# Kernel optimization log

Measured on AMD Instinct MI355X. Metric: run time of the kernel, lower is better.

## Reference

```python
import jax, jax.numpy as jnp
import numpy as np

B, L, D = 4, 2048, 512
N_HEAD, D_K, D_V = 8, 64, 64
D_INNER, N_LAYERS, NUM_TYPES = 2048, 4, 22
PAD = 0
LN_EPS = 1e-6


def _layer_norm(x, g, b):
    m = jnp.mean(x, axis=-1, keepdims=True)
    v = jnp.mean((x - m) ** 2, axis=-1, keepdims=True)
    return (x - m) * jax.lax.rsqrt(v + LN_EPS) * g + b


def _temporal_enc(time, non_pad_mask):
    # position_vec[i] = 10000^(2*(i//2)/d_model)
    i = np.arange(D)
    pos_vec = jnp.asarray(10000.0 ** (2.0 * (i // 2) / D), dtype=jnp.float32)
    r = time[:, :, None] / pos_vec                      # [B,L,D]
    even = (jnp.arange(D) % 2) == 0
    r = jnp.where(even, jnp.sin(r), jnp.cos(r))
    return r * non_pad_mask


def setup_inputs() -> dict:
    key = jax.random.key(0)
    ks = jax.random.split(key, 20)
    event_type = jax.random.randint(ks[0], (B, L), 0, NUM_TYPES + 1)
    event_time = jnp.cumsum(jax.random.uniform(ks[1], (B, L), dtype=jnp.float32), axis=1)
    non_pad_mask = (event_type != PAD).astype(jnp.float32)[:, :, None]
    s = 0.02
    emb = jax.random.normal(ks[2], (NUM_TYPES + 1, D), dtype=jnp.float32) * s
    emb = emb.at[PAD].set(0.0)  # padding_idx row
    Wq = jax.random.normal(ks[3], (N_LAYERS, D, N_HEAD * D_K), dtype=jnp.float32) * s
    Wk = jax.random.normal(ks[4], (N_LAYERS, D, N_HEAD * D_K), dtype=jnp.float32) * s
    Wv = jax.random.normal(ks[5], (N_LAYERS, D, N_HEAD * D_V), dtype=jnp.float32) * s
    fc_w = jax.random.normal(ks[6], (N_LAYERS, N_HEAD * D_V, D), dtype=jnp.float32) * s
    fc_b = jnp.zeros((N_LAYERS, D), dtype=jnp.float32)
    ln1_g = jnp.ones((N_LAYERS, D), dtype=jnp.float32)
    ln1_b = jnp.zeros((N_LAYERS, D), dtype=jnp.float32)
    W1 = jax.random.normal(ks[7], (N_LAYERS, D, D_INNER), dtype=jnp.float32) * s
    b1 = jnp.zeros((N_LAYERS, D_INNER), dtype=jnp.float32)
    W2 = jax.random.normal(ks[8], (N_LAYERS, D_INNER, D), dtype=jnp.float32) * s
    b2 = jnp.zeros((N_LAYERS, D), dtype=jnp.float32)
    ln2_g = jnp.ones((N_LAYERS, D), dtype=jnp.float32)
    ln2_b = jnp.zeros((N_LAYERS, D), dtype=jnp.float32)
    return dict(event_type=event_type, event_time=event_time, non_pad_mask=non_pad_mask,
                emb=emb, Wq=Wq, Wk=Wk, Wv=Wv, fc_w=fc_w, fc_b=fc_b,
                ln1_g=ln1_g, ln1_b=ln1_b, W1=W1, b1=b1, W2=W2, b2=b2,
                ln2_g=ln2_g, ln2_b=ln2_b)


def reference(event_type, event_time, non_pad_mask, emb, Wq, Wk, Wv, fc_w, fc_b,
              ln1_g, ln1_b, W1, b1, W2, b2, ln2_g, ln2_b):
    # Attention mask. NOTE: in the source, slf_attn_mask_sparse is overwritten by
    # the keypad mask, so the effective mask is padding | causal.
    pad = (event_type == PAD)                                   # [B,L]
    keypad = pad[:, None, :]                                    # [B,1(L_q),L_k] broadcast
    subseq = jnp.triu(jnp.ones((L, L), dtype=bool), k=1)        # [L,L]
    mask = (keypad | subseq)[:, None, :, :]                     # [B,1,L,L] over heads

    tem = _temporal_enc(event_time, non_pad_mask)               # [B,L,D]
    x = emb[event_type]                                         # [B,L,D]
    scale = 1.0 / jnp.sqrt(jnp.float32(D_K))

    for l in range(N_LAYERS):
        x = x + tem
        # --- multi-head attention (post-LN, THP style) ---
        residual = x
        q = (x @ Wq[l]).reshape(B, L, N_HEAD, D_K)
        k = (x @ Wk[l]).reshape(B, L, N_HEAD, D_K)
        v = (x @ Wv[l]).reshape(B, L, N_HEAD, D_V)
        scores = jnp.einsum('bqhd,bkhd->bhqk', q, k) * scale    # [B,H,L,L]
        scores = jnp.where(mask, -1e9, scores)
        attn = jax.nn.softmax(scores, axis=-1)
        out = jnp.einsum('bhqk,bkhd->bqhd', attn, v).reshape(B, L, N_HEAD * D_V)
        out = out @ fc_w[l] + fc_b[l] + residual
        x = _layer_norm(out, ln1_g[l], ln1_b[l])
        x = x * non_pad_mask
        # --- position-wise FFN (exact GELU, post-LN) ---
        residual = x
        h = jax.nn.gelu(x @ W1[l] + b1[l], approximate=False)
        y = h @ W2[l] + b2[l] + residual
        x = _layer_norm(y, ln2_g[l], ln2_b[l])
        x = x * non_pad_mask
    return x
```

## Files before the change

kernel.cpp:

```cpp
#include <hip/hip_runtime.h>
#include <math.h>

#define BB 4
#define LL 2048
#define DD 512
#define NH 8
#define DINNER 2048
#define NLAYERS 4
#define MM (BB * LL)

typedef __attribute__((ext_vector_type(8))) __bf16 bf16x8;
typedef __attribute__((ext_vector_type(4))) float f32x4;
typedef __attribute__((ext_vector_type(4))) unsigned short us4;

__device__ __forceinline__ unsigned short f2b(float f) {
  union { __bf16 h; unsigned short u; } v;
  v.h = (__bf16)f;
  return v.u;
}
__device__ __forceinline__ float b2f(unsigned short h) {
  union { unsigned u; float f; } v; v.u = ((unsigned)h) << 16; return v.f;
}
__device__ __forceinline__ unsigned pk2(float lo, float hi) {
  return (unsigned)f2b(lo) | ((unsigned)f2b(hi) << 16);
}
__device__ __forceinline__ float exp2f_fast(float x) {
  float r; asm("v_exp_f32 %0, %1" : "=v"(r) : "v"(x)); return r;
}

__device__ __forceinline__ void gload16(const void* g, void* l) {
  __builtin_amdgcn_global_load_lds(
      (const __attribute__((address_space(1))) void*)g,
      (__attribute__((address_space(3))) void*)l, 16, 0, 0);
}

__global__ __launch_bounds__(512) void init_kernel(
    const int* __restrict__ etype, const float* __restrict__ etime,
    const float* __restrict__ npm, const float* __restrict__ emb,
    float* __restrict__ tem, float* __restrict__ xa,
    unsigned short* __restrict__ xab) {
  int row = blockIdx.x;
  int d = threadIdx.x;
  float t = etime[row];
  float mask = npm[row];
  int dd = d & ~1;
  float pv = expf(9.210340371976184f * ((float)dd * (1.0f / (float)DD)));
  float r = t / pv;
  float val = (d & 1) ? cosf(r) : sinf(r);
  float tv = val * mask;
  tem[(size_t)row * DD + d] = tv;
  int ty = etype[row];
  float a = emb[(size_t)ty * DD + d] + tv;
  xa[(size_t)row * DD + d] = a;
  xab[(size_t)row * DD + d] = f2b(a);
}

__global__ __launch_bounds__(256) void wtrans_kernel(
    const float* __restrict__ in, unsigned short* __restrict__ out,
    int K, int N, long in_ls, long out_ls) {
  __shared__ float t[32][33];
  int l = blockIdx.z;
  int n0 = blockIdx.x * 32, k0 = blockIdx.y * 32;
  int tx = threadIdx.x & 31, ty = threadIdx.x >> 5;
  const float* ip = in + (size_t)l * in_ls;
  unsigned short* op = out + (size_t)l * out_ls;
#pragma unroll
  for (int r = ty; r < 32; r += 8)
    t[r][tx] = ip[(size_t)(k0 + r) * N + n0 + tx];
  __syncthreads();
#pragma unroll
  for (int r = ty; r < 32; r += 8)
    op[(size_t)(n0 + r) * K + k0 + tx] = f2b(t[tx][r]);
}

template <int BM, int BN, bool BIAS, bool RES, bool GELU_, bool OBF16>
__global__ __launch_bounds__(256) void gemm_kernel(
    const unsigned short* __restrict__ A, const unsigned short* __restrict__ WT,
    const float* __restrict__ bias, const float* __restrict__ res, int ldres,
    void* __restrict__ Cv, int ldc, int M, int N, int K) {
  __shared__ unsigned short As[2][BM * 32];
  __shared__ unsigned short Bs[2][BN * 32];
  constexpr int MT = (BM == 128) ? 4 : ((BN == 64) ? 2 : 4);
  constexpr int NT = (BM == 128 && BN == 128) ? 4 : 2;
  int tid = threadIdx.x;
  int w = tid >> 6, l = tid & 63;
  int li = l & 15, g = l >> 4;
  int nwg = gridDim.x;
  int bid = blockIdx.x;
  int wg = (bid & 7) * (nwg >> 3) + (bid >> 3);
  int gx = N / BN;
  int row0 = (wg / gx) * BM, col0 = (wg % gx) * BN;
  int wm = (BM == 128) ? (w & 1) * 64 : ((BN == 64) ? (w >> 1) * 32 : 0);
  int wnb = (BM == 128) ? (w >> 1) * 64 : ((BN == 64) ? (w & 1) * 32 : w * 32);
  f32x4 acc[MT][NT];
#pragma unroll
  for (int i = 0; i < MT; i++)
#pragma unroll
    for (int j = 0; j < NT; j++) acc[i][j] = (f32x4){0.f, 0.f, 0.f, 0.f};

  int lr = l >> 2;
  int lc = (l & 3) ^ (lr & 3);

  auto stage = [&](int bb, int kb) {
    int k0 = kb * 32;
    if (BM == 128) {
#pragma unroll
      for (int i = 0; i < 2; i++) {
        int ai = w * 2 + i;
        gload16(A + (size_t)(row0 + ai * 16 + lr) * K + k0 + lc * 8,
                &As[bb][ai * 512]);
      }
    } else {
      gload16(A + (size_t)(row0 + w * 16 + lr) * K + k0 + lc * 8,
              &As[bb][w * 512]);
    }
    if (BN == 128) {
#pragma unroll
      for (int i = 0; i < 2; i++) {
        int bi = w * 2 + i;
        gload16(WT + (size_t)(col0 + bi * 16 + lr) * K + k0 + lc * 8,
                &Bs[bb][bi * 512]);
      }
    } else {
      gload16(WT + (size_t)(col0 + w * 16 + lr) * K + k0 + lc * 8,
              &Bs[bb][w * 512]);
    }
  };

  int nk = K >> 5;
  stage(0, 0);
  __syncthreads();
  int buf = 0;
  for (int kb = 0; kb < nk; kb++) {
    if (kb + 1 < nk) stage(buf ^ 1, kb + 1);
    bf16x8 af[MT], bf_[NT];
#pragma unroll
    for (int mt = 0; mt < MT; mt++) {
      int r = wm + mt * 16 + li;
      af[mt] = *(const bf16x8*)&As[buf][r * 32 + ((g ^ (r & 3)) * 8)];
    }
#pragma unroll
    for (int nt = 0; nt < NT; nt++) {
      int r = wnb + nt * 16 + li;
      bf_[nt] = *(const bf16x8*)&Bs[buf][r * 32 + ((g ^ (r & 3)) * 8)];
    }
#pragma unroll
    for (int mt = 0; mt < MT; mt++)
#pragma unroll
      for (int nt = 0; nt < NT; nt++)
        acc[mt][nt] = __builtin_amdgcn_mfma_f32_16x16x32_bf16(
            af[mt], bf_[nt], acc[mt][nt], 0, 0, 0);
    __syncthreads();
    buf ^= 1;
  }
#pragma unroll
  for (int mt = 0; mt < MT; mt++) {
#pragma unroll
    for (int nt = 0; nt < NT; nt++) {
#pragma unroll
      for (int r = 0; r < 4; r++) {
        int row = row0 + wm + mt * 16 + g * 4 + r;
        int col = col0 + wnb + nt * 16 + li;
        float v = acc[mt][nt][r];
        if (BIAS) v += bias[col];
        if (RES) v += res[(size_t)row * ldres + col];
        if (GELU_) v = 0.5f * v * (1.0f + erff(v * 0.70710678118654752f));
        if (OBF16)
          ((unsigned short*)Cv)[(size_t)row * ldc + col] = f2b(v);
        else
          ((float*)Cv)[(size_t)row * ldc + col] = v;
      }
    }
  }
}

__global__ __launch_bounds__(256) void vtrans_kernel(
    const unsigned short* __restrict__ qkv, unsigned short* __restrict__ vT) {
  __shared__ unsigned short t[64][65];
  int bh = blockIdx.y;
  int b = bh >> 3, h = bh & 7;
  int l0 = blockIdx.x * 64;
  int tid = threadIdx.x;
  int c = tid & 63, p = tid >> 6;
#pragma unroll
  for (int r = p; r < 64; r += 4)
    t[r][c] = qkv[(size_t)(b * LL + l0 + r) * 1536 + 1024 + h * 64 + c];
  __syncthreads();
#pragma unroll
  for (int r = p; r < 64; r += 4)
    vT[((size_t)bh * 64 + r) * LL + l0 + c] = t[c][r];
}

__global__ __launch_bounds__(256) void meanv_kernel(
    const unsigned short* __restrict__ vT, float* __restrict__ meanVpart) {
  __shared__ float red[4][64];
  int chunk = blockIdx.x & 7;
  int bh = blockIdx.x >> 3;
  int tid = threadIdx.x;
  int d = tid & 63, p = tid >> 6;
  const unsigned short* vp =
      vT + ((size_t)bh * 64 + d) * LL + chunk * 256 + p * 64;
  float s = 0.f;
#pragma unroll
  for (int i = 0; i < 16; i++) {
    us4 v = *(const us4*)&vp[i * 4];
    s += b2f(v[0]) + b2f(v[1]) + b2f(v[2]) + b2f(v[3]);
  }
  red[p][d] = s;
  __syncthreads();
  if (p == 0)
    meanVpart[(size_t)blockIdx.x * 64 + d] =
        red[0][d] + red[1][d] + red[2][d] + red[3][d];
}

__global__ __launch_bounds__(256) void attn_kernel(
    const unsigned short* __restrict__ qkv, const unsigned short* __restrict__ vT,
    const int* __restrict__ etype, unsigned short* __restrict__ opart,
    float* __restrict__ ml) {
  __shared__ unsigned short Ks[2][64 * 64];
  __shared__ unsigned short Ps[64][72];
  int hwbid = blockIdx.x;
  int work = (hwbid & 7) * 256 + (hwbid >> 3);
  int bh = work >> 6;
  int rem = work & 63;
  int qt = 31 - (rem >> 1);
  int half = rem & 1;
  int h = bh & 7, b = bh >> 3;
  int q0 = qt * 64;
  int nt = qt + 1;
  int ha = (nt + 1) >> 1;
  int j0 = half ? ha : 0;
  int j1 = half ? nt : ha;
  int pidx = (bh * 32 + qt) * 2 + half;
  int tid = threadIdx.x, w = tid >> 6, l = tid & 63;
  int g = l >> 4, li = l & 15;
  const float SC = 0.125f * 1.44269504f;

  f32x4 o[4];
#pragma unroll
  for (int n = 0; n < 4; n++) o[n] = (f32x4){0.f, 0.f, 0.f, 0.f};
  float mreg[4], lreg[4];
#pragma unroll
  for (int r = 0; r < 4; r++) { mreg[r] = -3.0e38f; lreg[r] = 0.f; }

  if (j0 < j1) {
    const unsigned short* qrp =
        qkv + (size_t)(b * LL + q0 + w * 16 + li) * 1536 + h * 64;
    bf16x8 aq0 = *(const bf16x8*)&qrp[g * 8];
    bf16x8 aq1 = *(const bf16x8*)&qrp[32 + g * 8];

#pragma unroll
    for (int e = 0; e < 2; e++) {
      int idx = e * 256 + tid;
      int r = idx >> 3;
      int src = (l & 7) ^ (r & 7);
      gload16(
          qkv + (size_t)(b * LL + j0 * 64 + r) * 1536 + 512 + h * 64 + src * 8,
          &Ks[0][(e * 256 + w * 64) * 8]);
    }
    __syncthreads();

    int cur = 0;
    for (int j = j0; j < j1; j++) {
      int k0 = j << 6;
      if (j + 1 < j1) {
#pragma unroll
        for (int e = 0; e < 2; e++) {
          int idx = e * 256 + tid;
          int r = idx >> 3;
          int src = (l & 7) ^ (r & 7);
          gload16(qkv + (size_t)(b * LL + k0 + 64 + r) * 1536 + 512 + h * 64 +
                      src * 8,
                  &Ks[cur ^ 1][(e * 256 + w * 64) * 8]);
        }
      }
      bf16x8 bv0[4], bv1[4];
      float pb[4];
#pragma unroll
      for (int n = 0; n < 4; n++) {
        const unsigned short* vp =
            vT + ((size_t)(bh * 64 + n * 16 + li)) * LL + k0;
        bv0[n] = *(const bf16x8*)&vp[g * 8];
        bv1[n] = *(const bf16x8*)&vp[32 + g * 8];
        pb[n] = (etype[b * LL + k0 + n * 16 + li] == 0) ? -1.0e9f : 0.f;
      }
      f32x4 s[4];
#pragma unroll
      for (int n = 0; n < 4; n++) {
        int rK = n * 16 + li;
        const unsigned short* kb = &Ks[cur][rK * 64];
        bf16x8 bk0 = *(const bf16x8*)&kb[(g ^ (rK & 7)) * 8];
        bf16x8 bk1 = *(const bf16x8*)&kb[((g + 4) ^ (rK & 7)) * 8];
        f32x4 a = (f32x4){0.f, 0.f, 0.f, 0.f};
        __builtin_amdgcn_s_setprio(1);
        a = __builtin_amdgcn_mfma_f32_16x16x32_bf16(aq0, bk0, a, 0, 0, 0);
        a = __builtin_amdgcn_mfma_f32_16x16x32_bf16(aq1, bk1, a, 0, 0, 0);
        __builtin_amdgcn_s_setprio(0);
        s[n] = a;
      }
      if (j == qt) {
#pragma unroll
        for (int n = 0; n < 4; n++) {
          int key = k0 + n * 16 + li;
#pragma unroll
          for (int r = 0; r < 4; r++) {
            int qrow = q0 + w * 16 + g * 4 + r;
            float sv = fmaf(s[n][r], SC, pb[n]);
            if (key > qrow) sv = -1.0e9f;
            s[n][r] = sv;
          }
        }
      } else {
#pragma unroll
        for (int n = 0; n < 4; n++)
#pragma unroll
          for (int r = 0; r < 4; r++) s[n][r] = fmaf(s[n][r], SC, pb[n]);
      }
      float pm[4], corr[4], psum[4];
#pragma unroll
      for (int r = 0; r < 4; r++)
        pm[r] = fmaxf(fmaxf(s[0][r], s[1][r]), fmaxf(s[2][r], s[3][r]));
#pragma unroll
      for (int msk = 1; msk <= 8; msk <<= 1)
#pragma unroll
        for (int r = 0; r < 4; r++)
          pm[r] = fmaxf(pm[r], __shfl_xor(pm[r], msk, 64));
#pragma unroll
      for (int r = 0; r < 4; r++) {
        float mnew = fmaxf(mreg[r], pm[r]);
        corr[r] = exp2f_fast(mreg[r] - mnew);
        mreg[r] = mnew;
        float ps = 0.f;
#pragma unroll
        for (int n = 0; n < 4; n++) {
          float p = exp2f_fast(s[n][r] - mnew);
          s[n][r] = p;
          ps += p;
        }
        psum[r] = ps;
      }
#pragma unroll
      for (int msk = 1; msk <= 8; msk <<= 1)
#pragma unroll
        for (int r = 0; r < 4; r++) psum[r] += __shfl_xor(psum[r], msk, 64);
#pragma unroll
      for (int r = 0; r < 4; r++) lreg[r] = lreg[r] * corr[r] + psum[r];
#pragma unroll
      for (int n = 0; n < 4; n++)
#pragma unroll
        for (int r = 0; r < 4; r++)
          Ps[w * 16 + g * 4 + r][n * 16 + li] = f2b(s[n][r]);
#pragma unroll
      for (int n = 0; n < 4; n++)
#pragma unroll
        for (int r = 0; r < 4; r++) o[n][r] *= corr[r];
      bf16x8 ap0 = *(const bf16x8*)&Ps[w * 16 + li][g * 8];
      bf16x8 ap1 = *(const bf16x8*)&Ps[w * 16 + li][32 + g * 8];
      __builtin_amdgcn_s_setprio(1);
#pragma unroll
      for (int n = 0; n < 4; n++) {
        o[n] = __builtin_amdgcn_mfma_f32_16x16x32_bf16(ap0, bv0[n], o[n], 0, 0, 0);
        o[n] = __builtin_amdgcn_mfma_f32_16x16x32_bf16(ap1, bv1[n], o[n], 0, 0, 0);
      }
      __builtin_amdgcn_s_setprio(0);
      __syncthreads();
      cur ^= 1;
    }
  }
#pragma unroll
  for (int r = 0; r < 4; r++) {
    int qrl = w * 16 + g * 4 + r;
    float inv = (lreg[r] > 0.f) ? 1.0f / lreg[r] : 0.f;
#pragma unroll
    for (int n = 0; n < 4; n++)
      opart[((size_t)pidx * 64 + qrl) * 64 + n * 16 + li] = f2b(o[n][r] * inv);
    if (li == 0) {
      ml[(size_t)pidx * 128 + qrl] = mreg[r];
      ml[(size_t)pidx * 128 + 64 + qrl] = lreg[r];
    }
  }
}

__global__ __launch_bounds__(256) void amerge_kernel(
    const unsigned short* __restrict__ opart, const float* __restrict__ ml,
    const float* __restrict__ meanVpart, unsigned short* __restrict__ ao) {
  int blk = blockIdx.x;
  int bh = blk >> 5, qt = blk & 31;
  int b = bh >> 3, h = bh & 7;
  int tid = threadIdx.x;
  int d2 = (tid & 31) * 2;
  int pA = blk * 2, pB = blk * 2 + 1;
  for (int rr = tid >> 5; rr < 64; rr += 8) {
    float mA = ml[(size_t)pA * 128 + rr], lA = ml[(size_t)pA * 128 + 64 + rr];
    float mB = ml[(size_t)pB * 128 + rr], lB = ml[(size_t)pB * 128 + 64 + rr];
    float m = fmaxf(mA, mB);
    float v0, v1;
    if (m <= -1.0e8f) {
      float s0 = 0.f, s1 = 0.f;
#pragma unroll
      for (int cc = 0; cc < 8; cc++) {
        s0 += meanVpart[((size_t)bh * 8 + cc) * 64 + d2];
        s1 += meanVpart[((size_t)bh * 8 + cc) * 64 + d2 + 1];
      }
      v0 = s0 * (1.0f / (float)LL);
      v1 = s1 * (1.0f / (float)LL);
    } else {
      float a0 = 0.f, a1 = 0.f, wsum = 0.f;
      if (lA > 0.f) {
        float wA = exp2f_fast(mA - m) * lA;
        unsigned ua = *(const unsigned*)&opart[((size_t)pA * 64 + rr) * 64 + d2];
        a0 += b2f((unsigned short)ua) * wA;
        a1 += b2f((unsigned short)(ua >> 16)) * wA;
        wsum += wA;
      }
      if (lB > 0.f) {
        float wB = exp2f_fast(mB - m) * lB;
        unsigned ub = *(const unsigned*)&opart[((size_t)pB * 64 + rr) * 64 + d2];
        a0 += b2f((unsigned short)ub) * wB;
        a1 += b2f((unsigned short)(ub >> 16)) * wB;
        wsum += wB;
      }
      float inv = 1.0f / wsum;
      v0 = a0 * inv;
      v1 = a1 * inv;
    }
    int qr = qt * 64 + rr;
    *(unsigned*)&ao[(size_t)(b * LL + qr) * DD + h * 64 + d2] = pk2(v0, v1);
  }
}

template <bool ADDTEM>
__global__ __launch_bounds__(256) void ln_kernel(
    const unsigned short* __restrict__ in, const float* __restrict__ g,
    const float* __restrict__ bta, const float* __restrict__ npm,
    const float* __restrict__ tem, float* __restrict__ out,
    float* __restrict__ out2, unsigned short* __restrict__ out_bf) {
  __shared__ float red[4];
  int row = blockIdx.x;
  int tid = threadIdx.x;
  unsigned u = ((const unsigned*)(in + (size_t)row * DD))[tid];
  float v0 = b2f((unsigned short)u), v1 = b2f((unsigned short)(u >> 16));
  int e0 = tid * 2, e1 = tid * 2 + 1;
  float s = v0 + v1;
#pragma unroll
  for (int o = 32; o > 0; o >>= 1) s += __shfl_down(s, o, 64);
  if ((tid & 63) == 0) red[tid >> 6] = s;
  __syncthreads();
  float mean = (red[0] + red[1] + red[2] + red[3]) * (1.0f / (float)DD);
  float d0 = v0 - mean, d1 = v1 - mean;
  float sq = d0 * d0 + d1 * d1;
#pragma unroll
  for (int o = 32; o > 0; o >>= 1) sq += __shfl_down(sq, o, 64);
  __syncthreads();
  if ((tid & 63) == 0) red[tid >> 6] = sq;
  __syncthreads();
  float var = (red[0] + red[1] + red[2] + red[3]) * (1.0f / (float)DD);
  float rstd = rsqrtf(var + 1e-6f);
  float m = npm[row];
  float o0 = (d0 * rstd * g[e0] + bta[e0]) * m;
  float o1 = (d1 * rstd * g[e1] + bta[e1]) * m;
  ((float2*)(out + (size_t)row * DD))[tid] = make_float2(o0, o1);
  if (ADDTEM) {
    float2 tv = ((const float2*)(tem + (size_t)row * DD))[tid];
    float a0 = o0 + tv.x, a1 = o1 + tv.y;
    ((float2*)(out2 + (size_t)row * DD))[tid] = make_float2(a0, a1);
    ((unsigned*)(out_bf + (size_t)row * DD))[tid] = pk2(a0, a1);
  } else {
    ((unsigned*)(out_bf + (size_t)row * DD))[tid] = pk2(o0, o1);
  }
}

extern "C" void kernel_launch(void* const* d_in, const int* in_sizes, int n_in,
                              void* d_out, int out_size, void* d_ws,
                              size_t ws_size, hipStream_t stream) {
  const int* etype = (const int*)d_in[0];
  const float* etime = (const float*)d_in[1];
  const float* npm = (const float*)d_in[2];
  const float* emb = (const float*)d_in[3];
  const float* Wq = (const float*)d_in[4];
  const float* Wk = (const float*)d_in[5];
  const float* Wv = (const float*)d_in[6];
  const float* fc_w = (const float*)d_in[7];
  const float* fc_b = (const float*)d_in[8];
  const float* ln1_g = (const float*)d_in[9];
  const float* ln1_b = (const float*)d_in[10];
  const float* W1 = (const float*)d_in[11];
  const float* b1 = (const float*)d_in[12];
  const float* W2 = (const float*)d_in[13];
  const float* b2 = (const float*)d_in[14];
  const float* ln2_g = (const float*)d_in[15];
  const float* ln2_b = (const float*)d_in[16];

  float* x = (float*)d_out;
  char* ws = (char*)d_ws;
  const size_t SZF = (size_t)MM * DD * sizeof(float);
  const size_t SZB = (size_t)MM * DD * sizeof(short);
  float* tem = (float*)ws; ws += SZF;
  float* xa  = (float*)ws; ws += SZF;
  unsigned short* xab = (unsigned short*)ws; ws += SZB;
  unsigned short* xbf = (unsigned short*)ws; ws += SZB;
  unsigned short* qkv = (unsigned short*)ws; ws += (size_t)MM * 1536 * 2;
  unsigned short* vT  = (unsigned short*)ws; ws += (size_t)BB * NH * 64 * LL * 2;
  unsigned short* ao  = (unsigned short*)ws; ws += SZB;
  unsigned short* hb  = (unsigned short*)ws; ws += (size_t)MM * DINNER * 2;
  unsigned short* ybb = (unsigned short*)ws; ws += SZB;
  unsigned short* qkvT = (unsigned short*)ws; ws += (size_t)NLAYERS * 1536 * 512 * 2;
  unsigned short* fcT  = (unsigned short*)ws; ws += (size_t)NLAYERS * 512 * 512 * 2;
  unsigned short* W1T  = (unsigned short*)ws; ws += (size_t)NLAYERS * 2048 * 512 * 2;
  unsigned short* W2T  = (unsigned short*)ws; ws += (size_t)NLAYERS * 512 * 2048 * 2;
  float* meanVpart = (float*)ws; ws += (size_t)32 * 8 * 64 * sizeof(float);
  unsigned short* opart = (unsigned short*)ws; ws += (size_t)2048 * 64 * 64 * 2;
  float* ml = (float*)ws; ws += (size_t)2048 * 128 * sizeof(float);

  init_kernel<<<MM, 512, 0, stream>>>(etype, etime, npm, emb, tem, xa, xab);

  wtrans_kernel<<<dim3(16, 16, NLAYERS), 256, 0, stream>>>(
      Wq, qkvT + 0 * 512 * 512, 512, 512, 512L * 512, 1536L * 512);
  wtrans_kernel<<<dim3(16, 16, NLAYERS), 256, 0, stream>>>(
      Wk, qkvT + 1 * 512 * 512, 512, 512, 512L * 512, 1536L * 512);
  wtrans_kernel<<<dim3(16, 16, NLAYERS), 256, 0, stream>>>(
      Wv, qkvT + 2 * 512 * 512, 512, 512, 512L * 512, 1536L * 512);
  wtrans_kernel<<<dim3(16, 16, NLAYERS), 256, 0, stream>>>(
      fc_w, fcT, 512, 512, 512L * 512, 512L * 512);
  wtrans_kernel<<<dim3(64, 16, NLAYERS), 256, 0, stream>>>(
      W1, W1T, 512, 2048, 512L * 2048, 2048L * 512);
  wtrans_kernel<<<dim3(16, 64, NLAYERS), 256, 0, stream>>>(
      W2, W2T, 2048, 512, 2048L * 512, 512L * 2048);

  for (int l = 0; l < NLAYERS; l++) {
    gemm_kernel<128, 128, false, false, false, true><<<64 * 12, 256, 0, stream>>>(
        xab, qkvT + (size_t)l * 1536 * 512, nullptr, nullptr, 0, qkv, 1536,
        MM, 1536, 512);

    vtrans_kernel<<<dim3(32, 32), 256, 0, stream>>>(qkv, vT);
    meanv_kernel<<<32 * 8, 256, 0, stream>>>(vT, meanVpart);
    attn_kernel<<<2048, 256, 0, stream>>>(qkv, vT, etype, opart, ml);
    amerge_kernel<<<1024, 256, 0, stream>>>(opart, ml, meanVpart, ao);

    gemm_kernel<64, 64, true, true, false, true><<<128 * 8, 256, 0, stream>>>(
        ao, fcT + (size_t)l * 512 * 512, fc_b + (size_t)l * 512, xa, 512, ybb,
        512, MM, 512, 512);
    ln_kernel<false><<<MM, 256, 0, stream>>>(
        ybb, ln1_g + (size_t)l * 512, ln1_b + (size_t)l * 512, npm, nullptr, x,
        nullptr, xbf);

    gemm_kernel<128, 128, true, false, true, true><<<64 * 16, 256, 0, stream>>>(
        xbf, W1T + (size_t)l * 2048 * 512, b1 + (size_t)l * 2048, nullptr, 0,
        hb, 2048, MM, 2048, 512);
    gemm_kernel<64, 64, true, true, false, true><<<128 * 8, 256, 0, stream>>>(
        hb, W2T + (size_t)l * 512 * 2048, b2 + (size_t)l * 512, x, 512, ybb,
        512, MM, 512, 2048);
    if (l + 1 < NLAYERS) {
      ln_kernel<true><<<MM, 256, 0, stream>>>(
          ybb, ln2_g + (size_t)l * 512, ln2_b + (size_t)l * 512, npm, tem, x,
          xa, xab);
    } else {
      ln_kernel<false><<<MM, 256, 0, stream>>>(
          ybb, ln2_g + (size_t)l * 512, ln2_b + (size_t)l * 512, npm, nullptr,
          x, nullptr, xbf);
    }
  }
}
```

Before: 968.7 us.

## Cut redundant fp32 writes, use bf16 residual, vectorize V transpose, retile QKV GEMM

The layer-norm kernels now skip fp32 or bf16 outputs that no later kernel reads. The FFN second GEMM reads its residual from the bf16 copy instead of an fp32 buffer. The V transpose loads and stores four elements per thread, and the QKV projection GEMM moves from 128x128 to 64x128 tiles to launch more workgroups. Together these cut global memory traffic, but the bf16 residual adds rounding error to the FFN residual path.

```diff
diff --git a/kernel.cpp b/kernel.cpp
--- a/kernel.cpp
+++ b/kernel.cpp
@@ -73,10 +73,11 @@
     op[(size_t)(n0 + r) * K + k0 + tx] = f2b(t[tx][r]);
 }
 
-template <int BM, int BN, bool BIAS, bool RES, bool GELU_, bool OBF16>
+template <int BM, int BN, bool BIAS, bool RES, bool GELU_, bool OBF16,
+          bool RESB16>
 __global__ __launch_bounds__(256) void gemm_kernel(
     const unsigned short* __restrict__ A, const unsigned short* __restrict__ WT,
-    const float* __restrict__ bias, const float* __restrict__ res, int ldres,
+    const float* __restrict__ bias, const void* __restrict__ resv, int ldres,
     void* __restrict__ Cv, int ldc, int M, int N, int K) {
   __shared__ unsigned short As[2][BM * 32];
   __shared__ unsigned short Bs[2][BN * 32];
@@ -163,7 +164,12 @@
         int col = col0 + wnb + nt * 16 + li;
         float v = acc[mt][nt][r];
         if (BIAS) v += bias[col];
-        if (RES) v += res[(size_t)row * ldres + col];
+        if (RES) {
+          if (RESB16)
+            v += b2f(((const unsigned short*)resv)[(size_t)row * ldres + col]);
+          else
+            v += ((const float*)resv)[(size_t)row * ldres + col];
+        }
         if (GELU_) v = 0.5f * v * (1.0f + erff(v * 0.70710678118654752f));
         if (OBF16)
           ((unsigned short*)Cv)[(size_t)row * ldc + col] = f2b(v);
@@ -181,14 +187,24 @@
   int b = bh >> 3, h = bh & 7;
   int l0 = blockIdx.x * 64;
   int tid = threadIdx.x;
-  int c = tid & 63, p = tid >> 6;
-#pragma unroll
-  for (int r = p; r < 64; r += 4)
-    t[r][c] = qkv[(size_t)(b * LL + l0 + r) * 1536 + 1024 + h * 64 + c];
-  __syncthreads();
-#pragma unroll
-  for (int r = p; r < 64; r += 4)
-    vT[((size_t)bh * 64 + r) * LL + l0 + c] = t[c][r];
+  int rr = tid >> 4, c4 = (tid & 15) * 4;
+#pragma unroll
+  for (int pass = 0; pass < 4; pass++) {
+    int r = pass * 16 + rr;
+    us4 v = *(const us4*)&qkv[(size_t)(b * LL + l0 + r) * 1536 + 1024 +
+                              h * 64 + c4];
+    t[r][c4] = v[0];
+    t[r][c4 + 1] = v[1];
+    t[r][c4 + 2] = v[2];
+    t[r][c4 + 3] = v[3];
+  }
+  __syncthreads();
+#pragma unroll
+  for (int pass = 0; pass < 4; pass++) {
+    int r = pass * 16 + rr;
+    us4 v = {t[c4][r], t[c4 + 1][r], t[c4 + 2][r], t[c4 + 3][r]};
+    *(us4*)&vT[((size_t)bh * 64 + r) * LL + l0 + c4] = v;
+  }
 }
 
 __global__ __launch_bounds__(256) void meanv_kernel(
@@ -429,7 +445,7 @@
   }
 }
 
-template <bool ADDTEM>
+template <bool ADDTEM, bool WF32, bool WBF>
 __global__ __launch_bounds__(256) void ln_kernel(
     const unsigned short* __restrict__ in, const float* __restrict__ g,
     const float* __restrict__ bta, const float* __restrict__ npm,
@@ -459,13 +475,13 @@
   float m = npm[row];
   float o0 = (d0 * rstd * g[e0] + bta[e0]) * m;
   float o1 = (d1 * rstd * g[e1] + bta[e1]) * m;
-  ((float2*)(out + (size_t)row * DD))[tid] = make_float2(o0, o1);
+  if (WF32) ((float2*)(out + (size_t)row * DD))[tid] = make_float2(o0, o1);
   if (ADDTEM) {
     float2 tv = ((const float2*)(tem + (size_t)row * DD))[tid];
     float a0 = o0 + tv.x, a1 = o1 + tv.y;
     ((float2*)(out2 + (size_t)row * DD))[tid] = make_float2(a0, a1);
     ((unsigned*)(out_bf + (size_t)row * DD))[tid] = pk2(a0, a1);
-  } else {
+  } else if (WBF) {
     ((unsigned*)(out_bf + (size_t)row * DD))[tid] = pk2(o0, o1);
   }
 }
@@ -528,36 +544,40 @@
       W2, W2T, 2048, 512, 2048L * 512, 512L * 2048);
 
   for (int l = 0; l < NLAYERS; l++) {
-    gemm_kernel<128, 128, false, false, false, true><<<64 * 12, 256, 0, stream>>>(
-        xab, qkvT + (size_t)l * 1536 * 512, nullptr, nullptr, 0, qkv, 1536,
-        MM, 1536, 512);
+    gemm_kernel<64, 128, false, false, false, true, false>
+        <<<128 * 12, 256, 0, stream>>>(
+            xab, qkvT + (size_t)l * 1536 * 512, nullptr, nullptr, 0, qkv, 1536,
+            MM, 1536, 512);
 
     vtrans_kernel<<<dim3(32, 32), 256, 0, stream>>>(qkv, vT);
     meanv_kernel<<<32 * 8, 256, 0, stream>>>(vT, meanVpart);
     attn_kernel<<<2048, 256, 0, stream>>>(qkv, vT, etype, opart, ml);
     amerge_kernel<<<1024, 256, 0, stream>>>(opart, ml, meanVpart, ao);
 
-    gemm_kernel<64, 64, true, true, false, true><<<128 * 8, 256, 0, stream>>>(
-        ao, fcT + (size_t)l * 512 * 512, fc_b + (size_t)l * 512, xa, 512, ybb,
-        512, MM, 512, 512);
-    ln_kernel<false><<<MM, 256, 0, stream>>>(
-        ybb, ln1_g + (size_t)l * 512, ln1_b + (size_t)l * 512, npm, nullptr, x,
-        nullptr, xbf);
-
-    gemm_kernel<128, 128, true, false, true, true><<<64 * 16, 256, 0, stream>>>(
-        xbf, W1T + (size_t)l * 2048 * 512, b1 + (size_t)l * 2048, nullptr, 0,
-        hb, 2048, MM, 2048, 512);
-    gemm_kernel<64, 64, true, true, false, true><<<128 * 8, 256, 0, stream>>>(
-        hb, W2T + (size_t)l * 512 * 2048, b2 + (size_t)l * 512, x, 512, ybb,
-        512, MM, 512, 2048);
+    gemm_kernel<64, 64, true, true, false, true, false>
+        <<<128 * 8, 256, 0, stream>>>(
+            ao, fcT + (size_t)l * 512 * 512, fc_b + (size_t)l * 512, xa, 512,
+            ybb, 512, MM, 512, 512);
+    ln_kernel<false, false, true><<<MM, 256, 0, stream>>>(
+        ybb, ln1_g + (size_t)l * 512, ln1_b + (size_t)l * 512, npm, nullptr,
+        nullptr, nullptr, xbf);
+
+    gemm_kernel<128, 128, true, false, true, true, false>
+        <<<64 * 16, 256, 0, stream>>>(
+            xbf, W1T + (size_t)l * 2048 * 512, b1 + (size_t)l * 2048, nullptr,
+            0, hb, 2048, MM, 2048, 512);
+    gemm_kernel<64, 64, true, true, false, true, true>
+        <<<128 * 8, 256, 0, stream>>>(
+            hb, W2T + (size_t)l * 512 * 2048, b2 + (size_t)l * 512, xbf, 512,
+            ybb, 512, MM, 512, 2048);
     if (l + 1 < NLAYERS) {
-      ln_kernel<true><<<MM, 256, 0, stream>>>(
-          ybb, ln2_g + (size_t)l * 512, ln2_b + (size_t)l * 512, npm, tem, x,
-          xa, xab);
+      ln_kernel<true, false, false><<<MM, 256, 0, stream>>>(
+          ybb, ln2_g + (size_t)l * 512, ln2_b + (size_t)l * 512, npm, tem,
+          nullptr, xa, xab);
     } else {
-      ln_kernel<false><<<MM, 256, 0, stream>>>(
+      ln_kernel<false, true, false><<<MM, 256, 0, stream>>>(
           ybb, ln2_g + (size_t)l * 512, ln2_b + (size_t)l * 512, npm, nullptr,
-          x, nullptr, xbf);
-    }
-  }
-}
+          x, nullptr, nullptr);
+    }
+  }
+}
```

Result: no change. 957.0 us (-1.2%).
